# Optimization experiments

Hardware: AMD Instinct MI355X
Metric: run time of the kernel (lower is better)

Reference implementation:

```python
import jax, jax.numpy as jnp
import numpy as np

C1, C2 = 32, 16  # first_no_layer, second_no_layer
BN_EPS = 1e-5


def _irr(x, W, b):
    # Faithful port of irregular_convolution.forward.
    # x: [B, S, C, N, K] (torch layout with an extra seq axis).
    # torch: permute(0,1,3,2) then reshape([B, N, C*K]) -- a logical row-major
    # reshape of the transposed tensor (identical semantics in jnp).
    B, S, C, N, K = x.shape
    t = jnp.swapaxes(x, -1, -2).reshape(B, S, N, C * K)
    y = jnp.einsum('bsnm,om->bsno', t, W) + b  # tiny GEMM
    # permute(0,2,1).unsqueeze(-1) -> [B, S, O, N, 1]
    return jnp.moveaxis(y, -1, 2)[..., None]


def _prepare(y, neigh):
    # Faithful port of prepare_data: broadcast node row then masked_select.
    # y: [B, S, C, 1, N]; masked_select with a row-sorted kernel mask is a gather
    # of each node's sorted semantic neighbors: out[...,n,k] = y[...,0,neigh[n,k]].
    v = y[..., 0, :]          # [B, S, C, N]
    return v[..., neigh]      # [B, S, C, N, K]


def setup_inputs() -> dict:
    key = jax.random.key(0)
    ks = jax.random.split(key, 10)
    B, S, N, K = 8, 24, 4096, 9
    inp = {
        'input': jax.random.normal(ks[0], (B, S, N, K), dtype=jnp.float32),
        'neigh': jnp.sort(jax.random.randint(ks[1], (N, K), 0, N), axis=-1).astype(jnp.int32),
        'W1': jax.random.normal(ks[2], (C1, 1 * K), dtype=jnp.float32) * 0.05,
        'b1': jax.random.normal(ks[3], (C1,), dtype=jnp.float32) * 0.05,
        'W2': jax.random.normal(ks[4], (C2, C1 * K), dtype=jnp.float32) * 0.05,
        'b2': jax.random.normal(ks[5], (C2,), dtype=jnp.float32) * 0.05,
        'gamma': jnp.ones((C2,), dtype=jnp.float32),
        'beta': jnp.zeros((C2,), dtype=jnp.float32),
        'W3': jax.random.normal(ks[6], (1, C2 * K), dtype=jnp.float32) * 0.05,
        'b3': jax.random.normal(ks[7], (1,), dtype=jnp.float32) * 0.05,
    }
    return inp


def reference(input, neigh, W1, b1, W2, b2, gamma, beta, W3, b3):
    x = input[:, :, None]                                   # [B,S,1,N,K]
    h = jax.nn.relu(_irr(x, W1, b1))                        # [B,S,32,N,1]
    h = jnp.swapaxes(h, -1, -2)                             # [B,S,32,1,N]
    g = _prepare(h, neigh)                                  # [B,S,32,N,K]
    y = _irr(g, W2, b2)                                     # [B,S,16,N,1]
    # BatchNorm2d (training mode): stats over batch+spatial, per seq step & channel
    mean = jnp.mean(y, axis=(0, 3, 4), keepdims=True)
    var = jnp.var(y, axis=(0, 3, 4), keepdims=True)
    gb = (1, 1, C2, 1, 1)
    y = gamma.reshape(gb) * (y - mean) * jax.lax.rsqrt(var + BN_EPS) + beta.reshape(gb)
    y = jax.nn.relu(y)
    y = jnp.swapaxes(y, -1, -2)                             # [B,S,16,1,N]
    g = _prepare(y, neigh)                                  # [B,S,16,N,K]
    y = jax.nn.relu(_irr(g, W3, b3))                        # [B,S,1,N,1]
    return jnp.squeeze(y, axis=(2, 4))                      # [B,S,N]
```

## Files before the change

kernel.cpp:

```cpp
#include <hip/hip_runtime.h>
#include <hip/hip_bf16.h>

#define NB 8
#define NS 24
#define NN 4096
#define NC1 32
#define NC2 16
#define BN_COUNT 32768.0f

typedef float f32x4 __attribute__((ext_vector_type(4)));
typedef short bf16x8 __attribute__((ext_vector_type(8)));
union U8 { int4 i; bf16x8 b; };
union Q  { uint4 v; unsigned u[4]; };

#define PERM_LO 0x05040100u
#define PERM_HI 0x07060302u

__device__ __forceinline__ unsigned short bfbits(float x) {
    __hip_bfloat16 h = __float2bfloat16(x);
    return *(unsigned short*)&h;
}

__global__ __launch_bounds__(256) void k_prep(const float* __restrict__ input,
                                              float* __restrict__ flatT,
                                              const int* __restrict__ neigh,
                                              int* __restrict__ G2M,
                                              int* __restrict__ G3M,
                                              const float* __restrict__ W2,
                                              const float* __restrict__ W3,
                                              __hip_bfloat16* __restrict__ W2B,
                                              __hip_bfloat16* __restrict__ W3B) {
    __shared__ __align__(16) float tile[9216];
    int blk = blockIdx.x;
    if (blk >= 768) {
        int j = (blk - 768) * 256 + threadIdx.x;
        if (j < 36864) {
            int j8 = j & 7;
            int tkbl = j >> 3;
            int l = tkbl & 63;
            int tkb = tkbl >> 6;
            int t = tkb / 9, kb = tkb - t * 9;
            int r = t * 16 + (l & 15);
            int k = kb * 32 + ((l >> 4) << 3) + j8;
            int rem = r * 288 + k;
            G2M[j] = neigh[(rem & 4095) * 9 + (rem >> 12)];
        } else if (j < 77824) {
            int t2 = j - 36864;
            int j8 = t2 & 7;
            int tkbl = t2 >> 3;
            int l = tkbl & 63;
            int tkb = tkbl >> 6;
            int t = tkb / 5, kb = tkb - t * 5;
            int r = t * 16 + (l & 15);
            int k = kb * 32 + ((l >> 4) << 3) + j8;
            int rem = r * 144 + k;
            G3M[t2] = (k < 144) ? neigh[(rem & 4095) * 9 + (rem >> 12)] : 0;
        } else if (j < 82432) {
            int jj = j - 77824;
            int kb = jj >> 9;
            int rest = jj & 511;
            int l = rest >> 3, j8 = rest & 7;
            int o = l & 15;
            int k = kb * 32 + ((l >> 4) << 3) + j8;
            W2B[jj] = __float2bfloat16(W2[o * 288 + k]);
        } else {
            int jj = j - 82432;
            int kb = jj >> 9;
            int rest = jj & 511;
            int l = rest >> 3, j8 = rest & 7;
            int o = l & 15;
            int k = kb * 32 + ((l >> 4) << 3) + j8;
            W3B[jj] = __float2bfloat16((o == 0 && k < 144) ? W3[k] : 0.f);
        }
        return;
    }

    int tt = blk / 192;
    int bs = blk - tt * 192;
    int n0 = tt << 10;
    const float4* src = (const float4*)(input + (size_t)bs * 36864 + (size_t)n0 * 9);
    float4* tp = (float4*)tile;
    for (int j = threadIdx.x; j < 2304; j += 256) tp[j] = src[j];
    __syncthreads();
    float* dst = flatT + (size_t)bs * 36864 + n0;
    for (int j = threadIdx.x; j < 2304; j += 256) {
        int k = j >> 8, u = j & 255;
        float4 w;
        w.x = tile[(u * 4 + 0) * 9 + k];
        w.y = tile[(u * 4 + 1) * 9 + k];
        w.z = tile[(u * 4 + 2) * 9 + k];
        w.w = tile[(u * 4 + 3) * 9 + k];
        *(float4*)(dst + k * 4096 + u * 4) = w;
    }
}

__global__ __launch_bounds__(512, 4) void k_l12(const float* __restrict__ flatT,
                                                const float* __restrict__ W1,
                                                const float* __restrict__ b1,
                                                const int4* __restrict__ G2M4,
                                                const int4* __restrict__ W2B4,
                                                const float* __restrict__ b2,
                                                __hip_bfloat16* __restrict__ y2p,
                                                float* __restrict__ psum,
                                                float* __restrict__ psq) {
    __shared__ __align__(16) uint4 hl[4096];
    __shared__ float wred[2][8][16];
    int blk = blockIdx.x;
    int pl = blk / 192;
    int bs = blk - pl * 192;

    int tid = threadIdx.x;
    int l = tid & 63, w = tid >> 6;
    int o = l & 15, q = l >> 4;

    const int4* gp = G2M4 + (size_t)(w * 9) * 128 + l * 2;
    int4 ia = gp[0];
    int4 ib = gp[1];
    U8 bf; bf.i = W2B4[l];

    const float* T = flatT + (size_t)bs * 36864;
    const float* W1s = W1 + pl * 72;
    float b1v[8];
#pragma unroll
    for (int c = 0; c < 8; c++) b1v[c] = b1[pl * 8 + c];

#pragma unroll 2
    for (int j = 0; j < 8; j++) {
        int p = tid + 512 * j;
        const float* tp = T + p * 9;
        float v[9];
#pragma unroll
        for (int m = 0; m < 9; m++) v[m] = tp[m];
        uint4 d;
        unsigned* dp = (unsigned*)&d;
#pragma unroll
        for (int pr = 0; pr < 4; pr++) {
            float a0 = b1v[2 * pr], a1 = b1v[2 * pr + 1];
#pragma unroll
            for (int m = 0; m < 9; m++) a0 = fmaf(v[m], W1s[(2 * pr) * 9 + m], a0);
#pragma unroll
            for (int m = 0; m < 9; m++) a1 = fmaf(v[m], W1s[(2 * pr + 1) * 9 + m], a1);
            dp[pr] = (unsigned)bfbits(fmaxf(a0, 0.f)) |
                     ((unsigned)bfbits(fmaxf(a1, 0.f)) << 16);
        }
        hl[p] = d;
    }
    __syncthreads();

    float bb = b2[o];
    float s1 = 0.f, s2 = 0.f;
    __hip_bfloat16* ypl = y2p + (((size_t)(o >> 3) * 192 + bs) * NN) * 8 + (o & 7);

    f32x4 acc[8];
#pragma unroll
    for (int c = 0; c < 8; c++) acc[c] = (f32x4){0.f, 0.f, 0.f, 0.f};

#pragma unroll
    for (int kb = 0; kb < 9; kb++) {
        int4 na, nb; U8 nbf;
        if (kb < 8) {
            na = gp[(kb + 1) * 128];
            nb = gp[(kb + 1) * 128 + 1];
            nbf.i = W2B4[(kb + 1) * 64 + l];
        }
        Q d[8];
        d[0].v = hl[ia.x]; d[1].v = hl[ia.y]; d[2].v = hl[ia.z]; d[3].v = hl[ia.w];
        d[4].v = hl[ib.x]; d[5].v = hl[ib.y]; d[6].v = hl[ib.z]; d[7].v = hl[ib.w];
#pragma unroll
        for (int c = 0; c < 8; c++) {
            const int q2 = c >> 1;
            const unsigned sel = (c & 1) ? PERM_HI : PERM_LO;
            U8 Af;
            Af.i.x = __builtin_amdgcn_perm(d[1].u[q2], d[0].u[q2], sel);
            Af.i.y = __builtin_amdgcn_perm(d[3].u[q2], d[2].u[q2], sel);
            Af.i.z = __builtin_amdgcn_perm(d[5].u[q2], d[4].u[q2], sel);
            Af.i.w = __builtin_amdgcn_perm(d[7].u[q2], d[6].u[q2], sel);
            acc[c] = __builtin_amdgcn_mfma_f32_16x16x32_bf16(Af.b, bf.b, acc[c], 0, 0, 0);
        }
        if (kb < 8) { ia = na; ib = nb; bf = nbf; }
    }

    int rbase = w * 16 + q * 4;
#pragma unroll
    for (int c = 0; c < 8; c++) {
        int C = pl * 8 + c;
#pragma unroll
        for (int i = 0; i < 4; i++) {
            float v = acc[c][i] + bb;
            s1 += v; s2 += v * v;
            int n = C * 128 + rbase + i;
            ypl[(size_t)n * 8] = __float2bfloat16(v);
        }
    }

    s1 += __shfl_xor(s1, 16); s1 += __shfl_xor(s1, 32);
    s2 += __shfl_xor(s2, 16); s2 += __shfl_xor(s2, 32);
    if (l < 16) { wred[0][w][l] = s1; wred[1][w][l] = s2; }
    __syncthreads();
    if (tid < 16) {
        float a = 0.f, b = 0.f;
#pragma unroll
        for (int ww = 0; ww < 8; ww++) { a += wred[0][ww][tid]; b += wred[1][ww][tid]; }
        int srow = (bs % NS) * 16 + tid;
        int col  = (bs / NS) * 4 + pl;
        psum[srow * 32 + col] = a;
        psq [srow * 32 + col] = b;
    }
}

__global__ __launch_bounds__(512, 4) void k_l3bn(const uint4* __restrict__ y2p,
                                                 const int4* __restrict__ G3M4,
                                                 const int4* __restrict__ W3B4,
                                                 const float* __restrict__ psum,
                                                 const float* __restrict__ psq,
                                                 const float* __restrict__ gamma,
                                                 const float* __restrict__ beta,
                                                 const float* __restrict__ b3,
                                                 float* __restrict__ out) {
    __shared__ __align__(16) uint4 zl[4096];
    __shared__ float scl[8], shf[8];
    int blk = blockIdx.x;
    int bs = blk % 192;
    int oct = blk / 192;
    int s = bs % NS;
    int tid = threadIdx.x;

    if (tid < 256) {
        int jj = tid >> 5, col = tid & 31;
        int row = s * 16 + oct * 8 + jj;
        float sv = psum[row * 32 + col];
        float qv = psq [row * 32 + col];
        for (int off = 16; off; off >>= 1) {
            sv += __shfl_down(sv, off, 32);
            qv += __shfl_down(qv, off, 32);
        }
        if (col == 0) {
            float mean = sv * (1.0f / BN_COUNT);
            float var  = qv * (1.0f / BN_COUNT) - mean * mean;
            float inv  = rsqrtf(var + 1e-5f);
            int o = oct * 8 + jj;
            float scv = gamma[o] * inv;
            scl[jj] = scv;
            shf[jj] = beta[o] - mean * scv;
        }
    }
    __syncthreads();

    float sc[8], sh[8];
#pragma unroll
    for (int jj = 0; jj < 8; jj++) { sc[jj] = scl[jj]; sh[jj] = shf[jj]; }

    int l = tid & 63, w = tid >> 6;
    int o = l & 15, q = l >> 4;

    const int4* gp0 = G3M4 + (size_t)(w * 5) * 128 + l * 2;
    int4 ia = gp0[0];
    int4 ib = gp0[1];
    U8 bf; bf.i = W3B4[l];

    const uint4* yb = y2p + ((size_t)oct * 192 + bs) * NN;
#pragma unroll
    for (int jj = 0; jj < 8; jj++) {
        int j = tid + jj * 512;
        uint4 u = yb[j];
        unsigned r[4] = {u.x, u.y, u.z, u.w};
        uint4 pk;
        unsigned* pp = (unsigned*)&pk;
#pragma unroll
        for (int dd = 0; dd < 4; dd++) {
            float lo = fmaxf(fmaf(__uint_as_float(r[dd] << 16),         sc[dd*2],   sh[dd*2]),   0.f);
            float hi = fmaxf(fmaf(__uint_as_float(r[dd] & 0xffff0000u), sc[dd*2+1], sh[dd*2+1]), 0.f);
            unsigned ulo = __float_as_uint(lo) + 0x8000u;
            unsigned uhi = __float_as_uint(hi) + 0x8000u;
            pp[dd] = __builtin_amdgcn_perm(uhi, ulo, PERM_HI);
        }
        zl[j] = pk;
    }
    __syncthreads();

    float b3v = b3[0];

#pragma unroll
    for (int tt = 0; tt < 2; tt++) {
        int t = tt * 8 + w;
        const int4* gp = G3M4 + (size_t)(t * 5) * 128 + l * 2;
        f32x4 acc[8];
#pragma unroll
        for (int c = 0; c < 8; c++) acc[c] = (f32x4){0.f, 0.f, 0.f, 0.f};
#pragma unroll
        for (int kb = 0; kb < 5; kb++) {
            int4 na, nb; U8 nbf;
            if (kb < 4) {
                na = gp[(kb + 1) * 128];
                nb = gp[(kb + 1) * 128 + 1];
                nbf.i = W3B4[(kb + 1) * 64 + l];
            } else if (tt == 0) {
                const int4* gpn = G3M4 + (size_t)((8 + w) * 5) * 128 + l * 2;
                na = gpn[0];
                nb = gpn[1];
                nbf.i = W3B4[l];
            }
            Q d[8];
            d[0].v = zl[ia.x]; d[1].v = zl[ia.y]; d[2].v = zl[ia.z]; d[3].v = zl[ia.w];
            d[4].v = zl[ib.x]; d[5].v = zl[ib.y]; d[6].v = zl[ib.z]; d[7].v = zl[ib.w];
#pragma unroll
            for (int c = 0; c < 8; c++) {
                const int q2 = c >> 1;
                const unsigned sel = (c & 1) ? PERM_HI : PERM_LO;
                U8 Af;
                Af.i.x = __builtin_amdgcn_perm(d[1].u[q2], d[0].u[q2], sel);
                Af.i.y = __builtin_amdgcn_perm(d[3].u[q2], d[2].u[q2], sel);
                Af.i.z = __builtin_amdgcn_perm(d[5].u[q2], d[4].u[q2], sel);
                Af.i.w = __builtin_amdgcn_perm(d[7].u[q2], d[6].u[q2], sel);
                acc[c] = __builtin_amdgcn_mfma_f32_16x16x32_bf16(Af.b, bf.b, acc[c], 0, 0, 0);
            }
            if (kb < 4 || tt == 0) { ia = na; ib = nb; bf = nbf; }
        }
        if (o == 0) {
            int rbase = t * 16 + q * 4;
            float* ob = out + (size_t)bs * NN + oct * 2048;
#pragma unroll
            for (int c = 0; c < 8; c++) {
                float4 vv;
                vv.x = fmaxf(acc[c][0] + b3v, 0.f);
                vv.y = fmaxf(acc[c][1] + b3v, 0.f);
                vv.z = fmaxf(acc[c][2] + b3v, 0.f);
                vv.w = fmaxf(acc[c][3] + b3v, 0.f);
                *(float4*)(ob + c * 256 + rbase) = vv;
            }
        }
    }
}

extern "C" void kernel_launch(void* const* d_in, const int* in_sizes, int n_in,
                              void* d_out, int out_size, void* d_ws, size_t ws_size,
                              hipStream_t stream) {
    const float* input = (const float*)d_in[0];
    const int*   neigh = (const int*)d_in[1];
    const float* W1    = (const float*)d_in[2];
    const float* b1    = (const float*)d_in[3];
    const float* W2    = (const float*)d_in[4];
    const float* b2    = (const float*)d_in[5];
    const float* gamma = (const float*)d_in[6];
    const float* beta  = (const float*)d_in[7];
    const float* W3    = (const float*)d_in[8];
    const float* b3    = (const float*)d_in[9];
    float* out = (float*)d_out;

    char* ws = (char*)d_ws;
    int*            G2M   = (int*)            (ws);
    int*            G3M   = (int*)            (ws + 147456);
    __hip_bfloat16* W2B   = (__hip_bfloat16*) (ws + 311296);
    __hip_bfloat16* W3B   = (__hip_bfloat16*) (ws + 320512);
    float*          flatT = (float*)          (ws + 325632);
    __hip_bfloat16* y2    = (__hip_bfloat16*) (ws + 28637184);
    float*          psum  = (float*)          (ws + 53803008);
    float*          psq   = (float*)          (ws + 53852160);

    k_prep<<<1100, 256, 0, stream>>>(input, flatT, neigh, G2M, G3M,
                                     W2, W3, W2B, W3B);
    k_l12<<<768, 512, 0, stream>>>(flatT, W1, b1, (const int4*)G2M,
                                   (const int4*)W2B, b2, y2, psum, psq);
    k_l3bn<<<384, 512, 0, stream>>>((const uint4*)y2, (const int4*)G3M,
                                    (const int4*)W3B, psum, psq,
                                    gamma, beta, b3, out);
}
```

Measured before the change: 132.4 us.

## Vectorize layer-1 input loads, swizzle LDS layout, prefetch y2 before BN stats

The layer-1 compute loop now has each thread load four consecutive nodes' 9-float rows as nine 16-byte vector loads instead of scalar loads. The LDS writes and the gathered neighbor indices use a matching XOR-like swizzle, so the per-thread 4-node stores avoid bank conflicts. In the layer-3 kernel, the y2 tile, the gather indices and the weights are loaded into registers before the BN-statistics reduction and barrier, so global latency overlaps that reduction. This raises register pressure, and the swizzle must stay consistent between the index precompute and the LDS layout.

```diff
diff --git a/kernel.cpp b/kernel.cpp
--- a/kernel.cpp
+++ b/kernel.cpp
@@ -15,6 +15,8 @@
 
 #define PERM_LO 0x05040100u
 #define PERM_HI 0x07060302u
+
+#define SWZ(p) (((p) & ~3) | ((((p) & 3) + ((p) >> 3)) & 3))
 
 __device__ __forceinline__ unsigned short bfbits(float x) {
     __hip_bfloat16 h = __float2bfloat16(x);
@@ -43,7 +45,8 @@
             int r = t * 16 + (l & 15);
             int k = kb * 32 + ((l >> 4) << 3) + j8;
             int rem = r * 288 + k;
-            G2M[j] = neigh[(rem & 4095) * 9 + (rem >> 12)];
+            int v = neigh[(rem & 4095) * 9 + (rem >> 12)];
+            G2M[j] = SWZ(v);
         } else if (j < 77824) {
             int t2 = j - 36864;
             int j8 = t2 & 7;
@@ -124,26 +127,36 @@
 #pragma unroll
     for (int c = 0; c < 8; c++) b1v[c] = b1[pl * 8 + c];
 
-#pragma unroll 2
-    for (int j = 0; j < 8; j++) {
-        int p = tid + 512 * j;
-        const float* tp = T + p * 9;
-        float v[9];
-#pragma unroll
-        for (int m = 0; m < 9; m++) v[m] = tp[m];
-        uint4 d;
-        unsigned* dp = (unsigned*)&d;
-#pragma unroll
-        for (int pr = 0; pr < 4; pr++) {
-            float a0 = b1v[2 * pr], a1 = b1v[2 * pr + 1];
-#pragma unroll
-            for (int m = 0; m < 9; m++) a0 = fmaf(v[m], W1s[(2 * pr) * 9 + m], a0);
-#pragma unroll
-            for (int m = 0; m < 9; m++) a1 = fmaf(v[m], W1s[(2 * pr + 1) * 9 + m], a1);
-            dp[pr] = (unsigned)bfbits(fmaxf(a0, 0.f)) |
-                     ((unsigned)bfbits(fmaxf(a1, 0.f)) << 16);
-        }
-        hl[p] = d;
+#pragma unroll
+    for (int si = 0; si < 2; si++) {
+        int p0 = si * 2048 + tid * 4;
+        const f32x4* tp4 = (const f32x4*)(T + (size_t)p0 * 9);
+        f32x4 vv[9];
+#pragma unroll
+        for (int m = 0; m < 9; m++) vv[m] = tp4[m];
+#pragma unroll
+        for (int i = 0; i < 4; i++) {
+            uint4 d;
+            unsigned* dp = (unsigned*)&d;
+#pragma unroll
+            for (int pr = 0; pr < 4; pr++) {
+                float a0 = b1v[2 * pr], a1 = b1v[2 * pr + 1];
+#pragma unroll
+                for (int m = 0; m < 9; m++) {
+                    const int idx = i * 9 + m;
+                    a0 = fmaf(vv[idx >> 2][idx & 3], W1s[(2 * pr) * 9 + m], a0);
+                }
+#pragma unroll
+                for (int m = 0; m < 9; m++) {
+                    const int idx = i * 9 + m;
+                    a1 = fmaf(vv[idx >> 2][idx & 3], W1s[(2 * pr + 1) * 9 + m], a1);
+                }
+                dp[pr] = (unsigned)bfbits(fmaxf(a0, 0.f)) |
+                         ((unsigned)bfbits(fmaxf(a1, 0.f)) << 16);
+            }
+            int p = p0 + i;
+            hl[SWZ(p)] = d;
+        }
     }
     __syncthreads();
 
@@ -225,6 +238,18 @@
     int s = bs % NS;
     int tid = threadIdx.x;
 
+    const uint4* yb = y2p + ((size_t)oct * 192 + bs) * NN;
+    uint4 u[8];
+#pragma unroll
+    for (int jj = 0; jj < 8; jj++) u[jj] = yb[tid + jj * 512];
+
+    int l = tid & 63, w = tid >> 6;
+    int o = l & 15, q = l >> 4;
+    const int4* gp0 = G3M4 + (size_t)(w * 5) * 128 + l * 2;
+    int4 ia = gp0[0];
+    int4 ib = gp0[1];
+    U8 bf; bf.i = W3B4[l];
+
     if (tid < 256) {
         int jj = tid >> 5, col = tid & 31;
         int row = s * 16 + oct * 8 + jj;
@@ -238,10 +263,10 @@
             float mean = sv * (1.0f / BN_COUNT);
             float var  = qv * (1.0f / BN_COUNT) - mean * mean;
             float inv  = rsqrtf(var + 1e-5f);
-            int o = oct * 8 + jj;
-            float scv = gamma[o] * inv;
+            int oo = oct * 8 + jj;
+            float scv = gamma[oo] * inv;
             scl[jj] = scv;
-            shf[jj] = beta[o] - mean * scv;
+            shf[jj] = beta[oo] - mean * scv;
         }
     }
     __syncthreads();
@@ -250,20 +275,9 @@
 #pragma unroll
     for (int jj = 0; jj < 8; jj++) { sc[jj] = scl[jj]; sh[jj] = shf[jj]; }
 
-    int l = tid & 63, w = tid >> 6;
-    int o = l & 15, q = l >> 4;
-
-    const int4* gp0 = G3M4 + (size_t)(w * 5) * 128 + l * 2;
-    int4 ia = gp0[0];
-    int4 ib = gp0[1];
-    U8 bf; bf.i = W3B4[l];
-
-    const uint4* yb = y2p + ((size_t)oct * 192 + bs) * NN;
 #pragma unroll
     for (int jj = 0; jj < 8; jj++) {
-        int j = tid + jj * 512;
-        uint4 u = yb[j];
-        unsigned r[4] = {u.x, u.y, u.z, u.w};
+        unsigned r[4] = {u[jj].x, u[jj].y, u[jj].z, u[jj].w};
         uint4 pk;
         unsigned* pp = (unsigned*)&pk;
 #pragma unroll
@@ -274,7 +288,7 @@
             unsigned uhi = __float_as_uint(hi) + 0x8000u;
             pp[dd] = __builtin_amdgcn_perm(uhi, ulo, PERM_HI);
         }
-        zl[j] = pk;
+        zl[tid + jj * 512] = pk;
     }
     __syncthreads();
 
```

Measured after the change: 138.0 us. +4.3%, slower.
